# Kernel optimization log

Measured on AMD Instinct MI355X. Metric: run time of the kernel, lower is better.

The kernel has to match this reference:

```python
import jax, jax.numpy as jnp
import numpy as np

CAPACITY_FACTOR = 1.0


def setup_inputs() -> dict:
    key = jax.random.key(0)
    k = jax.random.split(key, 6)
    N, E, M, V = 8192, 8, 1024, 4096
    s = 0.02
    return {
        "x": jax.random.normal(k[0], (N, M), jnp.float32),
        "wg": jax.random.normal(k[1], (E, M), jnp.float32) * s,
        "fc1": jax.random.normal(k[2], (E, M, V), jnp.float32) * s,
        "b1": jax.random.normal(k[3], (E, V), jnp.float32) * s,
        "fc2": jax.random.normal(k[4], (E, V, M), jnp.float32) * s,
        "b2": jax.random.normal(k[5], (E, M), jnp.float32) * s,
    }


def reference(x, wg, fc1, b1, fc2, b2):
    N, M = x.shape
    E = wg.shape[0]
    capacity = 2 * int(CAPACITY_FACTOR * ((N + E - 1) // E))  # Top2 capacity

    # ---- Top2 gating ----
    logits = x @ wg.T                                   # [N, E]
    gates = jax.nn.softmax(logits, axis=1)
    _, top2 = jax.lax.top_k(logits, 2)                  # [N, 2]
    i1, i2 = top2[:, 0], top2[:, 1]
    m1 = jax.nn.one_hot(i1, E, dtype=jnp.int32)         # [N, E]
    m2 = jax.nn.one_hot(i2, E, dtype=jnp.int32)
    g1 = jnp.sum(gates * m1, axis=1)                    # [N]
    g2 = jnp.sum(gates * m2, axis=1)

    # cumulative-sum capacity assignment (per expert slot index)
    loc1 = jnp.cumsum(m1, axis=0) - 1                   # [N, E]
    loc2 = jnp.cumsum(m2, axis=0) - 1 + jnp.sum(m1, axis=0, keepdims=True)
    m1c = m1 * (loc1 < capacity).astype(jnp.int32)
    m2c = m2 * (loc2 < capacity).astype(jnp.int32)
    loc1_s = jnp.sum(loc1 * m1c, axis=1)                # [N]
    loc2_s = jnp.sum(loc2 * m2c, axis=1)
    v1 = jnp.sum(m1c, axis=1)                           # 0/1 kept flags
    v2 = jnp.sum(m2c, axis=1)

    # aux load-balancing loss (fp32 branch of original)
    me = jnp.sum(gates, axis=0)
    ce = jnp.sum(m1c.astype(gates.dtype), axis=0)
    l_aux = jnp.sum(me * ce) * (E / (N * N))

    # ---- dispatch (scatter tokens into [E*C, M]) ----
    idx1 = jnp.where(v1 > 0, i1 * capacity + loc1_s, -1)
    idx2 = jnp.where(v2 > 0, i2 * capacity + loc2_s, -1)
    disp = jnp.zeros((E * capacity, M), x.dtype)
    disp = disp.at[idx1].add(x, mode="drop")
    disp = disp.at[idx2].add(x, mode="drop")

    # ---- fused FFN experts ----
    d = disp.reshape(E, capacity, M)
    h = jnp.einsum("ecm,emv->ecv", d, fc1) + b1[:, None, :]
    h = jax.nn.relu(h)
    y = jnp.einsum("ecv,evm->ecm", h, fc2) + b2[:, None, :]
    yf = y.reshape(E * capacity, M)

    # ---- combine (gather + gate-weighted sum) ----
    v1f = v1.astype(x.dtype)
    v2f = v2.astype(x.dtype)
    out = (g1 * v1f)[:, None] * yf[i1 * capacity + loc1_s] \
        + (g2 * v2f)[:, None] * yf[i2 * capacity + loc2_s]
    return out, l_aux
```

## Files before the change

kernel.cpp:

```cpp
#include <hip/hip_runtime.h>
#include <stdint.h>

typedef __attribute__((ext_vector_type(8))) short short8;
typedef __attribute__((ext_vector_type(4))) float f32x4;

#define N_TOK 8192
#define E_EXP 8
#define M_DIM 1024
#define V_DIM 4096
#define CAP   2048
#define SLOTS (E_EXP*CAP)

__device__ __forceinline__ unsigned short f2bf(float f){
  unsigned u = __float_as_uint(f);
  u += 0x7FFFu + ((u >> 16) & 1u);
  return (unsigned short)(u >> 16);
}

__device__ __forceinline__ void gload_lds16(const void* g, void* l){
  __builtin_amdgcn_global_load_lds(
    (const __attribute__((address_space(1))) void*)g,
    (__attribute__((address_space(3))) void*)l, 16, 0, 0);
}

__global__ __launch_bounds__(256) void routing_kernel(
    const float* __restrict__ x, const float* __restrict__ wg,
    float* __restrict__ gates, int* __restrict__ i1o, int* __restrict__ i2o,
    float* __restrict__ g1o, float* __restrict__ g2o)
{
  int wv = threadIdx.x >> 6, lane = threadIdx.x & 63;
  int n = blockIdx.x * 4 + wv;
  const float* xr = x + (size_t)n * M_DIM;
  double acc[8];
  #pragma unroll
  for (int e = 0; e < 8; e++) acc[e] = 0.0;
  for (int j = 0; j < M_DIM/64; j++){
    double xv = (double)xr[lane + j*64];
    #pragma unroll
    for (int e = 0; e < 8; e++) acc[e] += xv * (double)wg[e*M_DIM + lane + j*64];
  }
  #pragma unroll
  for (int off = 32; off > 0; off >>= 1){
    #pragma unroll
    for (int e = 0; e < 8; e++) acc[e] += __shfl_down(acc[e], off);
  }
  if (lane == 0){
    float lg[8], mx = -1e30f;
    #pragma unroll
    for (int e = 0; e < 8; e++){ lg[e] = (float)acc[e]; mx = fmaxf(mx, lg[e]); }
    float s = 0.f, gt[8];
    #pragma unroll
    for (int e = 0; e < 8; e++){ gt[e] = expf(lg[e] - mx); s += gt[e]; }
    float inv = 1.f / s;
    int i1 = 0;
    #pragma unroll
    for (int e = 1; e < 8; e++) if (lg[e] > lg[i1]) i1 = e;
    int i2 = (i1 == 0) ? 1 : 0;
    #pragma unroll
    for (int e = 0; e < 8; e++){ if (e == i1) continue; if (lg[e] > lg[i2]) i2 = e; }
    #pragma unroll
    for (int e = 0; e < 8; e++) gates[(size_t)n*8 + e] = gt[e] * inv;
    i1o[n] = i1; i2o[n] = i2;
    g1o[n] = gt[i1] * inv; g2o[n] = gt[i2] * inv;
  }
}

__global__ __launch_bounds__(1024) void scan_kernel(
    const int* __restrict__ i1, const int* __restrict__ i2,
    int* __restrict__ s1, int* __restrict__ s2, int* __restrict__ ce_out)
{
  __shared__ unsigned long long sc[4][1024];
  const int t = threadIdx.x;
  int e1l[8], e2l[8];
  unsigned long long c[4] = {0ull,0ull,0ull,0ull};
  #pragma unroll
  for (int k = 0; k < 8; k++){
    int a = i1[t*8+k]; e1l[k] = a; c[a>>2]       += 1ull << ((a&3)*16);
    int b = i2[t*8+k]; e2l[k] = b; c[2 + (b>>2)] += 1ull << ((b&3)*16);
  }
  #pragma unroll
  for (int i = 0; i < 4; i++) sc[i][t] = c[i];
  __syncthreads();
  for (int st = 1; st < 1024; st <<= 1){
    unsigned long long add[4];
    #pragma unroll
    for (int i = 0; i < 4; i++) add[i] = (t >= st) ? sc[i][t-st] : 0ull;
    __syncthreads();
    #pragma unroll
    for (int i = 0; i < 4; i++) if (t >= st) sc[i][t] += add[i];
    __syncthreads();
  }
  unsigned long long ex[4], tot[4];
  #pragma unroll
  for (int i = 0; i < 4; i++){ ex[i] = sc[i][t] - c[i]; tot[i] = sc[i][1023]; }
  int r1[8], r2[8], t1[8];
  #pragma unroll
  for (int e = 0; e < 8; e++){
    r1[e] = (int)((ex[e>>2]       >> ((e&3)*16)) & 0xFFFF);
    r2[e] = (int)((ex[2 + (e>>2)] >> ((e&3)*16)) & 0xFFFF);
    t1[e] = (int)((tot[e>>2]      >> ((e&3)*16)) & 0xFFFF);
  }
  #pragma unroll
  for (int k = 0; k < 8; k++){
    int n = t*8 + k;
    int a = e1l[k]; int loc1 = r1[a]++;
    s1[n] = (loc1 < CAP) ? (a*CAP + loc1) : -1;
    int b = e2l[k]; int loc2 = r2[b]++ + t1[b];
    s2[n] = (loc2 < CAP) ? (b*CAP + loc2) : -1;
  }
  if (t == 0){
    #pragma unroll
    for (int e = 0; e < 8; e++) ce_out[e] = (t1[e] < CAP) ? t1[e] : CAP;
  }
}

__global__ __launch_bounds__(1024) void laux_kernel(
    const float* __restrict__ gates, const int* __restrict__ ce, float* __restrict__ dst)
{
  __shared__ float red[1024];
  const int t = threadIdx.x;
  float part[8];
  #pragma unroll
  for (int e = 0; e < 8; e++) part[e] = 0.f;
  for (int k = 0; k < 8; k++){
    int n = t + k*1024;
    #pragma unroll
    for (int e = 0; e < 8; e++) part[e] += gates[(size_t)n*8 + e];
  }
  float laux = 0.f;
  for (int e = 0; e < 8; e++){
    red[t] = part[e];
    __syncthreads();
    for (int s = 512; s > 0; s >>= 1){ if (t < s) red[t] += red[t+s]; __syncthreads(); }
    if (t == 0) laux += red[0] * (float)ce[e];
    __syncthreads();
  }
  if (t == 0) dst[0] = laux * (float)(8.0/(8192.0*8192.0));
}

__global__ void build_droplist(const int* __restrict__ s1, const int* __restrict__ s2,
                               int* __restrict__ list, int* __restrict__ cnt)
{
  int lane = threadIdx.x;
  int base = 0;
  int a = s1[lane], b = s2[lane];
  for (int it = 0; it < N_TOK/64; it++){
    int na = 0, nb = 0;
    if (it + 1 < N_TOK/64){
      na = s1[(it+1)*64 + lane];
      nb = s2[(it+1)*64 + lane];
    }
    int n = it*64 + lane;
    bool f1 = (a == -1) || (a == SLOTS-1);
    unsigned long long m1 = __ballot(f1);
    if (f1) list[base + __popcll(m1 & ((1ull<<lane)-1))] = n;
    base += __popcll(m1);
    bool f2 = (b == -1) || (b == SLOTS-1);
    unsigned long long m2 = __ballot(f2);
    if (f2) list[base + __popcll(m2 & ((1ull<<lane)-1))] = n;
    base += __popcll(m2);
    a = na; b = nb;
  }
  if (lane == 0) *cnt = base;
}

__global__ void dropacc1_kernel(const float* __restrict__ x, const int* __restrict__ list,
                                const int* __restrict__ cnt, float* __restrict__ partial)
{
  int col = blockIdx.x*256 + threadIdx.x;
  int sl  = blockIdx.y;
  int c = *cnt;
  int per = (c + 15) >> 4;
  int lo = sl*per, hi = lo + per; if (hi > c) hi = c;
  float a = 0.f;
  for (int i = lo; i < hi; i++) a += x[(size_t)list[i]*M_DIM + col];
  partial[sl*M_DIM + col] = a;
}
__global__ void dropacc2_kernel(const float* __restrict__ partial, float* __restrict__ drow)
{
  int col = blockIdx.x*256 + threadIdx.x;
  float s = 0.f;
  #pragma unroll
  for (int j = 0; j < 16; j++) s += partial[j*M_DIM + col];
  drow[col] = s;
}

template<bool RELU>
__global__ __launch_bounds__(256) void fix_gemv(
    const float* __restrict__ vec, const float* __restrict__ W,
    const float* __restrict__ bias, float* __restrict__ outv, int K, int N)
{
  __shared__ float red[256];
  const int o = threadIdx.x & 15;
  const int c = threadIdx.x >> 4;
  const int n = blockIdx.x*16 + o;
  const int chunk = K >> 4;
  float a = 0.f;
  for (int k = c*chunk; k < (c+1)*chunk; k++) a += vec[k] * W[(size_t)k*N + n];
  red[threadIdx.x] = a;
  __syncthreads();
  if (c == 0){
    float s = 0.f;
    #pragma unroll
    for (int j = 0; j < 16; j++) s += red[o + j*16];
    s += bias[n];
    if (RELU) s = fmaxf(s, 0.f);
    outv[n] = s;
  }
}

__global__ void scatter_kernel(const float* __restrict__ x, const int* __restrict__ s1,
                               const int* __restrict__ s2, unsigned short* __restrict__ dispB,
                               int e0, int epb)
{
  int n = blockIdx.x, t = threadIdx.x;
  int a = s1[n], b = s2[n];
  int za = (a >= 0) ? (a >> 11) - e0 : -1;
  int zb = (b >= 0) ? (b >> 11) - e0 : -1;
  bool wa = (za >= 0) && (za < epb);
  bool wb = (zb >= 0) && (zb < epb);
  if (!wa && !wb) return;
  const float4 v = *(const float4*)(x + (size_t)n*M_DIM + t*4);
  ushort4 o;
  o.x = f2bf(v.x); o.y = f2bf(v.y); o.z = f2bf(v.z); o.w = f2bf(v.w);
  if (wa) *(ushort4*)(dispB + ((size_t)za*CAP + (a & (CAP-1)))*M_DIM + t*4) = o;
  if (wb) *(ushort4*)(dispB + ((size_t)zb*CAP + (b & (CAP-1)))*M_DIM + t*4) = o;
}

__global__ __launch_bounds__(256) void transpose_f32_bf16(
    const float* __restrict__ in, unsigned short* __restrict__ out,
    int R, int C, size_t estride)
{
  __shared__ float tile[32][33];
  const size_t eo = (size_t)blockIdx.z * estride;
  int c0 = blockIdx.x*32, r0 = blockIdx.y*32;
  int tx = threadIdx.x & 31, ty = threadIdx.x >> 5;
  #pragma unroll
  for (int j = 0; j < 4; j++)
    tile[ty + j*8][tx] = in[eo + (size_t)(r0 + ty + j*8)*C + (c0 + tx)];
  __syncthreads();
  #pragma unroll
  for (int j = 0; j < 4; j++)
    out[eo + (size_t)(c0 + ty + j*8)*R + (r0 + tx)] = f2bf(tile[tx][ty + j*8]);
}

template<bool RELU_BF16>
__global__ __launch_bounds__(512, 2) void gemm_tn(
    const unsigned short* __restrict__ A, size_t aE,
    const unsigned short* __restrict__ B, size_t bE,
    const float* __restrict__ bias, size_t biasE,
    void* __restrict__ outp, size_t oE, int K, int Ncols, int gx, int gy)
{
  __shared__ unsigned short As[3][256*32];
  __shared__ unsigned short Bs[3][256*32];
  const int nwg = gridDim.x;
  const int orig = blockIdx.x;
  const int wgid = (orig & 7) * (nwg >> 3) + (orig >> 3);
  const int z  = wgid / (gx*gy);
  const int rr = wgid - z*gx*gy;
  const int by = rr / gx, bx = rr - by*gx;

  const unsigned short* Ae = A + (size_t)z * aE;
  const unsigned short* Be = B + (size_t)z * bE;
  const float* be = bias + (size_t)z * biasE;
  const int row0 = by * 256;
  const int col0 = bx * 256;
  const int tid = threadIdx.x;
  const int lane = tid & 63, wv = tid >> 6;
  const int wr = wv >> 2, wc = wv & 3;
  const int frow = lane & 15, fq = lane >> 4;

  f32x4 acc[8][4];
  #pragma unroll
  for (int i = 0; i < 8; i++)
    #pragma unroll
    for (int j = 0; j < 4; j++) acc[i][j] = (f32x4){0.f,0.f,0.f,0.f};

  auto STAGE_A = [&](int buf, int k0){
    #pragma unroll
    for (int i = 0; i < 2; i++){
      int cb = i*512 + wv*64;
      int c  = cb + lane;
      int r  = c >> 2;
      int gs = (c & 3) ^ ((r >> 1) & 3);
      gload_lds16(Ae + (size_t)(row0 + r)*K + (k0 + gs*8), &As[buf][cb*8]);
    }
  };
  auto STAGE_B = [&](int buf, int k0){
    #pragma unroll
    for (int i = 0; i < 2; i++){
      int cb = i*512 + wv*64;
      int c  = cb + lane;
      int r  = c >> 2;
      int gs = (c & 3) ^ ((r >> 1) & 3);
      gload_lds16(Be + (size_t)(col0 + r)*K + (k0 + gs*8), &Bs[buf][cb*8]);
    }
  };

  const int nt = K >> 5;
  STAGE_A(0, 0);  STAGE_B(0, 0);
  STAGE_A(1, 32); STAGE_B(1, 32);
  asm volatile("s_waitcnt vmcnt(4)" ::: "memory");
  __builtin_amdgcn_sched_barrier(0);
  __builtin_amdgcn_s_barrier();

  for (int t = 0; t < nt; ++t){
    const int buf = t % 3;
    const int nb  = (t + 2) % 3;
    const int nk  = (t + 2) * 32;
    short8 af0[4], af1[4], bfv[4];
    #pragma unroll
    for (int f = 0; f < 4; f++){
      int row = wr*128 + f*16 + frow;
      int sl  = fq ^ ((row >> 1) & 3);
      af0[f] = *(const short8*)&As[buf][row*32 + sl*8];
    }
    #pragma unroll
    for (int f = 0; f < 4; f++){
      int row = wc*64 + f*16 + frow;
      int sl  = fq ^ ((row >> 1) & 3);
      bfv[f] = *(const short8*)&Bs[buf][row*32 + sl*8];
    }
    if (t + 2 < nt) STAGE_A(nb, nk);
    __builtin_amdgcn_s_setprio(1);
    #pragma unroll
    for (int fm = 0; fm < 4; fm++)
      #pragma unroll
      for (int fn = 0; fn < 4; fn++)
        acc[fm][fn] = __builtin_amdgcn_mfma_f32_16x16x32_bf16(af0[fm], bfv[fn], acc[fm][fn], 0, 0, 0);
    __builtin_amdgcn_s_setprio(0);
    __builtin_amdgcn_s_barrier();
    #pragma unroll
    for (int f = 0; f < 4; f++){
      int row = wr*128 + (4+f)*16 + frow;
      int sl  = fq ^ ((row >> 1) & 3);
      af1[f] = *(const short8*)&As[buf][row*32 + sl*8];
    }
    if (t + 2 < nt) STAGE_B(nb, nk);
    __builtin_amdgcn_s_setprio(1);
    #pragma unroll
    for (int fm = 0; fm < 4; fm++)
      #pragma unroll
      for (int fn = 0; fn < 4; fn++)
        acc[4+fm][fn] = __builtin_amdgcn_mfma_f32_16x16x32_bf16(af1[fm], bfv[fn], acc[4+fm][fn], 0, 0, 0);
    __builtin_amdgcn_s_setprio(0);
    if (t + 1 < nt){
      if (t + 2 < nt){
        asm volatile("s_waitcnt vmcnt(4)" ::: "memory");
      } else {
        asm volatile("s_waitcnt vmcnt(0)" ::: "memory");
      }
      __builtin_amdgcn_sched_barrier(0);
      __builtin_amdgcn_s_barrier();
    }
  }

  const int rsub = fq * 4;
  #pragma unroll
  for (int fn = 0; fn < 4; fn++){
    int col = col0 + wc*64 + fn*16 + frow;
    float bv = be[col];
    #pragma unroll
    for (int fm = 0; fm < 8; fm++){
      int row = row0 + wr*128 + fm*16 + rsub;
      #pragma unroll
      for (int r = 0; r < 4; r++){
        float v = acc[fm][fn][r] + bv;
        if (RELU_BF16){
          v = fmaxf(v, 0.f);
          ((unsigned short*)outp)[(size_t)z*oE + (size_t)(row + r)*Ncols + col] = f2bf(v);
        } else {
          ((float*)outp)[(size_t)z*oE + (size_t)(row + r)*Ncols + col] = v;
        }
      }
    }
  }
}

__global__ void gather_full_kernel(const float* __restrict__ y, const int* __restrict__ s1,
    const int* __restrict__ s2, const float* __restrict__ g1, const float* __restrict__ g2,
    float* __restrict__ out)
{
  int n = blockIdx.x, t = threadIdx.x;
  int a = s1[n], b = s2[n];
  float c1 = (a >= 0) ? g1[n] : 0.f; int p1 = (a >= 0) ? a : 0;
  float c2 = (b >= 0) ? g2[n] : 0.f; int p2 = (b >= 0) ? b : 0;
  const float4 v1 = *(const float4*)(y + (size_t)p1*M_DIM + t*4);
  const float4 v2 = *(const float4*)(y + (size_t)p2*M_DIM + t*4);
  float4 o;
  o.x = c1*v1.x + c2*v2.x; o.y = c1*v1.y + c2*v2.y;
  o.z = c1*v1.z + c2*v2.z; o.w = c1*v1.w + c2*v2.w;
  *(float4*)(out + (size_t)n*M_DIM + t*4) = o;
}

__global__ void gather_kernel(const float* __restrict__ yB, const int* __restrict__ s1,
    const int* __restrict__ s2, const float* __restrict__ g1, const float* __restrict__ g2,
    float* __restrict__ out, int e0, int epb)
{
  int n = blockIdx.x, t = threadIdx.x;
  int a = s1[n], b = s2[n];
  float4 o;
  bool touched = false;
  for (int z = 0; z < epb; z++){
    int e = e0 + z;
    float coef = 0.f; int loc = 0; bool m = false;
    if (a >= 0 && (a >> 11) == e){ coef = g1[n]; loc = a & (CAP-1); m = true; }
    else if (b >= 0 && (b >> 11) == e){ coef = g2[n]; loc = b & (CAP-1); m = true; }
    if (m){
      if (!touched) o = *(const float4*)(out + (size_t)n*M_DIM + t*4);
      const float4 v = *(const float4*)(yB + ((size_t)z*CAP + loc)*M_DIM + t*4);
      o.x += coef*v.x; o.y += coef*v.y; o.z += coef*v.z; o.w += coef*v.w;
      touched = true;
    }
  }
  if (touched) *(float4*)(out + (size_t)n*M_DIM + t*4) = o;
}

extern "C" void kernel_launch(void* const* d_in, const int* in_sizes, int n_in,
                              void* d_out, int out_size, void* d_ws, size_t ws_size,
                              hipStream_t stream)
{
  const float* x   = (const float*)d_in[0];
  const float* wg  = (const float*)d_in[1];
  const float* fc1 = (const float*)d_in[2];
  const float* b1  = (const float*)d_in[3];
  const float* fc2 = (const float*)d_in[4];
  const float* b2  = (const float*)d_in[5];
  float* out = (float*)d_out;
  char* ws = (char*)d_ws;

  size_t off = 0;
  auto take = [&](size_t b)->char*{ char* p = ws + off; off += (b + 255) & ~(size_t)255; return p; };

  float* gates = (float*)take((size_t)N_TOK*8*4);
  int*   i1    = (int*)  take((size_t)N_TOK*4);
  int*   i2    = (int*)  take((size_t)N_TOK*4);
  float* g1    = (float*)take((size_t)N_TOK*4);
  float* g2    = (float*)take((size_t)N_TOK*4);
  int*   s1    = (int*)  take((size_t)N_TOK*4);
  int*   s2    = (int*)  take((size_t)N_TOK*4);
  int*   ce    = (int*)  take(256);
  int*   list  = (int*)  take((size_t)2*N_TOK*4);
  int*   cnt   = (int*)  take(256);
  float* dpart = (float*)take((size_t)16*M_DIM*4);
  float* drow  = (float*)take((size_t)M_DIM*4);
  float* hrow  = (float*)take((size_t)V_DIM*4);

  const size_t perExp = (size_t)CAP*M_DIM*2
                      + (size_t)M_DIM*V_DIM*2*2
                      + (size_t)CAP*V_DIM*2
                      + (size_t)CAP*M_DIM*4;
  int epb = 0;
  {
    const int cands[3] = {8, 4, 2};
    for (int ci = 0; ci < 3; ci++){
      if (off + (size_t)cands[ci]*perExp + (1u<<20) <= ws_size){ epb = cands[ci]; break; }
    }
  }
  if (!epb){
    hipMemsetAsync(d_out, 0, (size_t)out_size*4, stream);
    return;
  }
  unsigned short* dispB = (unsigned short*)take((size_t)epb*CAP*M_DIM*2);
  unsigned short* fc1bB = (unsigned short*)take((size_t)epb*M_DIM*V_DIM*2);
  unsigned short* fc2bB = (unsigned short*)take((size_t)epb*M_DIM*V_DIM*2);
  unsigned short* hB    = (unsigned short*)take((size_t)epb*CAP*V_DIM*2);
  float*          yB    = (float*)         take((size_t)epb*CAP*M_DIM*4);

  routing_kernel<<<N_TOK/4, 256, 0, stream>>>(x, wg, gates, i1, i2, g1, g2);
  scan_kernel<<<1, 1024, 0, stream>>>(i1, i2, s1, s2, ce);
  laux_kernel<<<1, 1024, 0, stream>>>(gates, ce, out + (size_t)N_TOK*M_DIM);
  if (epb < 8) hipMemsetAsync(out, 0, (size_t)N_TOK*M_DIM*4, stream);
  build_droplist<<<1, 64, 0, stream>>>(s1, s2, list, cnt);
  dropacc1_kernel<<<dim3(4,16), 256, 0, stream>>>(x, list, cnt, dpart);
  dropacc2_kernel<<<4, 256, 0, stream>>>(dpart, drow);

  const size_t eW = (size_t)M_DIM*V_DIM;
  for (int e0 = 0; e0 < E_EXP; e0 += epb){
    scatter_kernel<<<N_TOK, 256, 0, stream>>>(x, s1, s2, dispB, e0, epb);
    transpose_f32_bf16<<<dim3(V_DIM/32, M_DIM/32, epb), 256, 0, stream>>>(fc1 + (size_t)e0*eW, fc1bB, M_DIM, V_DIM, eW);
    transpose_f32_bf16<<<dim3(M_DIM/32, V_DIM/32, epb), 256, 0, stream>>>(fc2 + (size_t)e0*eW, fc2bB, V_DIM, M_DIM, eW);
    gemm_tn<true ><<<(V_DIM/256)*(CAP/256)*epb, 512, 0, stream>>>(
        dispB, (size_t)CAP*M_DIM, fc1bB, eW, b1 + (size_t)e0*V_DIM, V_DIM,
        hB, (size_t)CAP*V_DIM, M_DIM, V_DIM, V_DIM/256, CAP/256);
    gemm_tn<false><<<(M_DIM/256)*(CAP/256)*epb, 512, 0, stream>>>(
        hB, (size_t)CAP*V_DIM, fc2bB, eW, b2 + (size_t)e0*M_DIM, M_DIM,
        yB, (size_t)CAP*M_DIM, V_DIM, M_DIM, M_DIM/256, CAP/256);
    if (E_EXP-1 >= e0 && E_EXP-1 < e0+epb){
      fix_gemv<true ><<<V_DIM/16, 256, 0, stream>>>(drow, fc1 + (size_t)(E_EXP-1)*eW, b1 + (size_t)(E_EXP-1)*V_DIM, hrow, M_DIM, V_DIM);
      fix_gemv<false><<<M_DIM/16, 256, 0, stream>>>(hrow, fc2 + (size_t)(E_EXP-1)*eW, b2 + (size_t)(E_EXP-1)*M_DIM,
                                                    yB + ((size_t)(E_EXP-1-e0)*CAP + (CAP-1))*M_DIM, V_DIM, M_DIM);
    }
    if (epb < 8)
      gather_kernel<<<N_TOK, 256, 0, stream>>>(yB, s1, s2, g1, g2, out, e0, epb);
  }
  if (epb == 8)
    gather_full_kernel<<<N_TOK, 256, 0, stream>>>(yB, s1, s2, g1, g2, out);
}
```

Measured before the change: 684.5 us.

## Switch GEMM mainloop to BK=64 double-buffered tiles with four-phase MFMA schedule

The bf16 GEMM mainloop moves from a triple-buffered K=32 pipeline to a double-buffered K=64 tile with an 8-way XOR swizzle. Each iteration now runs four MFMA quadrants, and the next tile's B and A loads are issued into the current buffer once its fragments are in registers. The aim is to halve the number of loop iterations and barriers per K and to hide global-to-LDS traffic behind more MFMA work. In exchange there is less prefetch depth, more fragment registers, and an in-place reload of the buffer that relies on the barrier ordering being correct.

```diff
diff --git a/kernel.cpp b/kernel.cpp
--- a/kernel.cpp
+++ b/kernel.cpp
@@ -251,8 +251,8 @@
     const float* __restrict__ bias, size_t biasE,
     void* __restrict__ outp, size_t oE, int K, int Ncols, int gx, int gy)
 {
-  __shared__ unsigned short As[3][256*32];
-  __shared__ unsigned short Bs[3][256*32];
+  __shared__ unsigned short As[2][256*64];
+  __shared__ unsigned short Bs[2][256*64];
   const int nwg = gridDim.x;
   const int orig = blockIdx.x;
   const int wgid = (orig & 7) * (nwg >> 3) + (orig >> 3);
@@ -276,77 +276,113 @@
     #pragma unroll
     for (int j = 0; j < 4; j++) acc[i][j] = (f32x4){0.f,0.f,0.f,0.f};
 
-  auto STAGE_A = [&](int buf, int k0){
+  auto STAGE = [&](unsigned short* lds, const unsigned short* gsrc, int base0, int half, int k0){
     #pragma unroll
     for (int i = 0; i < 2; i++){
       int cb = i*512 + wv*64;
       int c  = cb + lane;
-      int r  = c >> 2;
-      int gs = (c & 3) ^ ((r >> 1) & 3);
-      gload_lds16(Ae + (size_t)(row0 + r)*K + (k0 + gs*8), &As[buf][cb*8]);
+      int r  = c >> 3, s = c & 7;
+      gload_lds16(gsrc + (size_t)(base0 + half*128 + r)*K + (k0 + ((s ^ (r & 7))*8)),
+                  lds + half*8192 + cb*8);
     }
   };
-  auto STAGE_B = [&](int buf, int k0){
-    #pragma unroll
-    for (int i = 0; i < 2; i++){
-      int cb = i*512 + wv*64;
-      int c  = cb + lane;
-      int r  = c >> 2;
-      int gs = (c & 3) ^ ((r >> 1) & 3);
-      gload_lds16(Be + (size_t)(col0 + r)*K + (k0 + gs*8), &Bs[buf][cb*8]);
-    }
-  };
-
-  const int nt = K >> 5;
-  STAGE_A(0, 0);  STAGE_B(0, 0);
-  STAGE_A(1, 32); STAGE_B(1, 32);
-  asm volatile("s_waitcnt vmcnt(4)" ::: "memory");
+
+  const int nt = K >> 6;
+  STAGE(&As[0][0], Ae, row0, 0, 0);  STAGE(&As[0][0], Ae, row0, 1, 0);
+  STAGE(&Bs[0][0], Be, col0, 0, 0);  STAGE(&Bs[0][0], Be, col0, 1, 0);
+  STAGE(&As[1][0], Ae, row0, 0, 64); STAGE(&As[1][0], Ae, row0, 1, 64);
+  STAGE(&Bs[1][0], Be, col0, 0, 64); STAGE(&Bs[1][0], Be, col0, 1, 64);
+  asm volatile("s_waitcnt vmcnt(0)" ::: "memory");
   __builtin_amdgcn_sched_barrier(0);
   __builtin_amdgcn_s_barrier();
 
+  short8 a[8], bA[4], bB[4];
   for (int t = 0; t < nt; ++t){
-    const int buf = t % 3;
-    const int nb  = (t + 2) % 3;
-    const int nk  = (t + 2) * 32;
-    short8 af0[4], af1[4], bfv[4];
-    #pragma unroll
-    for (int f = 0; f < 4; f++){
-      int row = wr*128 + f*16 + frow;
-      int sl  = fq ^ ((row >> 1) & 3);
-      af0[f] = *(const short8*)&As[buf][row*32 + sl*8];
-    }
-    #pragma unroll
-    for (int f = 0; f < 4; f++){
-      int row = wc*64 + f*16 + frow;
-      int sl  = fq ^ ((row >> 1) & 3);
-      bfv[f] = *(const short8*)&Bs[buf][row*32 + sl*8];
-    }
-    if (t + 2 < nt) STAGE_A(nb, nk);
+    const int buf = t & 1;
+    const int nk  = (t + 2) << 6;
+    const bool st = (t + 2) < nt;
+    #pragma unroll
+    for (int fm = 0; fm < 4; fm++)
+      #pragma unroll
+      for (int ks = 0; ks < 2; ks++){
+        int row = wr*128 + fm*16 + frow;
+        int sl  = (ks*4 + fq) ^ (row & 7);
+        a[fm*2+ks] = *(const short8*)&As[buf][row*64 + sl*8];
+      }
+    #pragma unroll
+    for (int fn = 0; fn < 2; fn++)
+      #pragma unroll
+      for (int ks = 0; ks < 2; ks++){
+        int col = wc*64 + fn*16 + frow;
+        int sl  = (ks*4 + fq) ^ (col & 7);
+        bA[fn*2+ks] = *(const short8*)&Bs[buf][col*64 + sl*8];
+      }
     __builtin_amdgcn_s_setprio(1);
     #pragma unroll
     for (int fm = 0; fm < 4; fm++)
       #pragma unroll
-      for (int fn = 0; fn < 4; fn++)
-        acc[fm][fn] = __builtin_amdgcn_mfma_f32_16x16x32_bf16(af0[fm], bfv[fn], acc[fm][fn], 0, 0, 0);
+      for (int fn = 0; fn < 2; fn++)
+        #pragma unroll
+        for (int ks = 0; ks < 2; ks++)
+          acc[fm][fn] = __builtin_amdgcn_mfma_f32_16x16x32_bf16(a[fm*2+ks], bA[fn*2+ks], acc[fm][fn], 0, 0, 0);
     __builtin_amdgcn_s_setprio(0);
     __builtin_amdgcn_s_barrier();
     #pragma unroll
-    for (int f = 0; f < 4; f++){
-      int row = wr*128 + (4+f)*16 + frow;
-      int sl  = fq ^ ((row >> 1) & 3);
-      af1[f] = *(const short8*)&As[buf][row*32 + sl*8];
-    }
-    if (t + 2 < nt) STAGE_B(nb, nk);
+    for (int fn = 0; fn < 2; fn++)
+      #pragma unroll
+      for (int ks = 0; ks < 2; ks++){
+        int col = wc*64 + (2+fn)*16 + frow;
+        int sl  = (ks*4 + fq) ^ (col & 7);
+        bB[fn*2+ks] = *(const short8*)&Bs[buf][col*64 + sl*8];
+      }
     __builtin_amdgcn_s_setprio(1);
     #pragma unroll
     for (int fm = 0; fm < 4; fm++)
       #pragma unroll
-      for (int fn = 0; fn < 4; fn++)
-        acc[4+fm][fn] = __builtin_amdgcn_mfma_f32_16x16x32_bf16(af1[fm], bfv[fn], acc[4+fm][fn], 0, 0, 0);
+      for (int fn = 0; fn < 2; fn++)
+        #pragma unroll
+        for (int ks = 0; ks < 2; ks++)
+          acc[fm][2+fn] = __builtin_amdgcn_mfma_f32_16x16x32_bf16(a[fm*2+ks], bB[fn*2+ks], acc[fm][2+fn], 0, 0, 0);
+    __builtin_amdgcn_s_setprio(0);
+    __builtin_amdgcn_s_barrier();
+    #pragma unroll
+    for (int fm = 0; fm < 4; fm++)
+      #pragma unroll
+      for (int ks = 0; ks < 2; ks++){
+        int row = wr*128 + (4+fm)*16 + frow;
+        int sl  = (ks*4 + fq) ^ (row & 7);
+        a[fm*2+ks] = *(const short8*)&As[buf][row*64 + sl*8];
+      }
+    if (st){
+      STAGE(&Bs[buf][0], Be, col0, 0, nk);
+      STAGE(&Bs[buf][0], Be, col0, 1, nk);
+    }
+    __builtin_amdgcn_s_setprio(1);
+    #pragma unroll
+    for (int fm = 0; fm < 4; fm++)
+      #pragma unroll
+      for (int fn = 0; fn < 2; fn++)
+        #pragma unroll
+        for (int ks = 0; ks < 2; ks++)
+          acc[4+fm][fn] = __builtin_amdgcn_mfma_f32_16x16x32_bf16(a[fm*2+ks], bA[fn*2+ks], acc[4+fm][fn], 0, 0, 0);
+    __builtin_amdgcn_s_setprio(0);
+    __builtin_amdgcn_s_barrier();
+    if (st){
+      STAGE(&As[buf][0], Ae, row0, 0, nk);
+      STAGE(&As[buf][0], Ae, row0, 1, nk);
+    }
+    __builtin_amdgcn_s_setprio(1);
+    #pragma unroll
+    for (int fm = 0; fm < 4; fm++)
+      #pragma unroll
+      for (int fn = 0; fn < 2; fn++)
+        #pragma unroll
+        for (int ks = 0; ks < 2; ks++)
+          acc[4+fm][2+fn] = __builtin_amdgcn_mfma_f32_16x16x32_bf16(a[fm*2+ks], bB[fn*2+ks], acc[4+fm][2+fn], 0, 0, 0);
     __builtin_amdgcn_s_setprio(0);
     if (t + 1 < nt){
-      if (t + 2 < nt){
-        asm volatile("s_waitcnt vmcnt(4)" ::: "memory");
+      if (st){
+        asm volatile("s_waitcnt vmcnt(8)" ::: "memory");
       } else {
         asm volatile("s_waitcnt vmcnt(0)" ::: "memory");
       }
```

Result: faster. 670.0 us (-2.1%).
